# Kernel tuning notes

Measured on AMD Instinct MI355X. Metric: run time of the kernel, lower is better.

## Reference

```python
import jax, jax.numpy as jnp
import numpy as np

N_PTS = 8192   # collocation points (original used 50; scaled up)
N_PARA = 5000  # rows of para, matching the source script
HID = 50


def setup_inputs() -> dict:
    key = jax.random.key(0)
    ks = jax.random.split(key, 10)
    x = jax.random.normal(ks[0], (N_PTS, 3), jnp.float32)
    # para = cat(normal(-2,1) [P,2], normal(0.5,1) [P,1]) as in source script
    a_b = jax.random.normal(ks[1], (N_PARA, 2), jnp.float32) * 1.0 - 2.0
    c = jax.random.normal(ks[2], (N_PARA, 1), jnp.float32) * 1.0 + 0.5
    para = jnp.concatenate([a_b, c], axis=1)

    def init(k, fan_in, shape):
        bound = 1.0 / np.sqrt(fan_in)  # torch Linear default init range
        return jax.random.uniform(k, shape, jnp.float32, -bound, bound)

    W_in = init(ks[3], 3, (3, HID))
    b_in = init(ks[4], 3, (HID,))
    W_hid = init(ks[5], HID, (4, HID, HID))
    b_hid = init(ks[6], HID, (4, HID))
    W_out = init(ks[7], HID, (HID, 2))
    b_out = init(ks[8], HID, (2,))
    return dict(x=x, para=para, W_in=W_in, b_in=b_in, W_hid=W_hid,
                b_hid=b_hid, W_out=W_out, b_out=b_out)


def reference(x, para, W_in, b_in, W_hid, b_hid, W_out, b_out):
    def net(xi):  # xi: [3] -> [2] (u, v)
        h = jnp.tanh(xi @ W_in + b_in)
        for i in range(W_hid.shape[0]):
            h = jnp.tanh(h @ W_hid[i] + b_hid[i])
        return h @ W_out + b_out

    uv = jax.vmap(net)(x)                    # [N, 2]
    jac = jax.vmap(jax.jacrev(net))(x)       # [N, 2, 3]
    hess = jax.vmap(jax.hessian(net))(x)     # [N, 2, 3, 3]

    u, v = uv[:, 0], uv[:, 1]
    u_t, v_t = jac[:, 0, 2], jac[:, 1, 2]
    u_xx, u_yy = hess[:, 0, 0, 0], hess[:, 0, 1, 1]
    v_xx, v_yy = hess[:, 1, 0, 0], hess[:, 1, 1, 1]

    Q = u * u + v * v  # |q|^2
    # f_2 = u_t + 0.5 v_xx + 0.5 a v_yy - 0.5 u_yy + Q v - Q c u + u
    # f_1 = v_t - 0.5 u_xx - 0.5 a u_yy - 0.5 v_yy - Q u - Q c v + v
    base2 = u_t + 0.5 * v_xx - 0.5 * u_yy + Q * v + u   # a,c-independent part
    base1 = v_t - 0.5 * u_xx - 0.5 * v_yy - Q * u + v

    a = para[:, 0:1]   # [P, 1]; column 1 (b) is unused, as in source
    cc = para[:, 2:3]

    f1 = base1[None, :] - 0.5 * a * u_yy[None, :] - cc * (Q * v)[None, :]  # [P, N]
    f2 = base2[None, :] + 0.5 * a * v_yy[None, :] - cc * (Q * u)[None, :]

    # per-row loss: MSE(f1, 0) + MSE(f2, 0)
    return jnp.mean(f1 * f1, axis=1) + jnp.mean(f2 * f2, axis=1)  # [P]
```

## Files before the change

kernel.cpp:

```cpp
#include <hip/hip_runtime.h>
#include <math.h>

#define HID 50
#define NPTS 8192
#define NPARA 5000
#define NLAYERS 4

typedef float f32x4 __attribute__((ext_vector_type(4)));
typedef short short8 __attribute__((ext_vector_type(8)));

union U4S8 { uint4 u; short8 s; };

#define WS_PART 0
#define WS_FRAG 32768
#define WS_WIN  98304
#define WS_BIN  99072
#define WS_BH   99328
#define WS_WOUT 100352
#define WS_NEED 100864

#define S_STRIDE 21
#define S_COMP   (64*S_STRIDE)
#define S_WORDS  (6*S_COMP)

__device__ __forceinline__ float fast_tanh(float x) {
    const float ax = __builtin_fabsf(x);
    const float e  = __expf(2.0f * ax);
    const float r  = __builtin_amdgcn_rcpf(e + 1.0f);
    const float t  = fmaf(-2.0f, r, 1.0f);
    return __builtin_copysignf(t, x);
}

__device__ __forceinline__ void split_bf16(float x, unsigned &hi, unsigned &lo) {
    const unsigned u = __float_as_uint(x);
    const unsigned h = u & 0xFFFF0000u;
    const float rem  = x - __uint_as_float(h);
    const unsigned r = __float_as_uint(rem);
    hi = h >> 16;
    lo = (r + 0x7FFFu + ((r >> 16) & 1u)) >> 16;
}

__device__ __forceinline__ uint4 pack8(const unsigned v[8]) {
    return make_uint4(v[0] | (v[1] << 16), v[2] | (v[3] << 16),
                      v[4] | (v[5] << 16), v[6] | (v[7] << 16));
}

__global__ __launch_bounds__(256) void prep_kernel(
    const float* __restrict__ W_in, const float* __restrict__ b_in,
    const float* __restrict__ W_hid, const float* __restrict__ b_hid,
    const float* __restrict__ W_out, char* __restrict__ wsbase)
{
    const int gid = blockIdx.x * 256 + threadIdx.x;
    if (gid < 2048) {
        const int fid = gid >> 6, lane = gid & 63;
        const int l = fid >> 3, c = (fid >> 2) & 1, t = fid & 3;
        const int q = lane >> 4, n = lane & 15;
        const int gn = t*16 + n;
        unsigned hi[8], lo[8];
        #pragma unroll
        for (int jj = 0; jj < 8; ++jj) {
            const int k = c*32 + q*8 + jj;
            const float w = (k < HID && gn < HID) ? W_hid[(l*HID + k)*HID + gn] : 0.f;
            split_bf16(w, hi[jj], lo[jj]);
        }
        uint4* frag = (uint4*)(wsbase + WS_FRAG);
        frag[(fid*2 + 0)*64 + lane] = pack8(hi);
        frag[(fid*2 + 1)*64 + lane] = pack8(lo);
    } else if (gid < 2240) {
        const int i = gid - 2048, d = i >> 6, j = i & 63;
        ((float*)(wsbase + WS_WIN))[i] = (j < HID) ? W_in[d*HID + j] : 0.f;
    } else if (gid < 2304) {
        const int j = gid - 2240;
        ((float*)(wsbase + WS_BIN))[j] = (j < HID) ? b_in[j] : 0.f;
    } else if (gid < 2560) {
        const int i = gid - 2304, l = i >> 6, j = i & 63;
        ((float*)(wsbase + WS_BH))[i] = (j < HID) ? b_hid[l*HID + j] : 0.f;
    } else if (gid < 2688) {
        const int i = gid - 2560, j = i >> 1, s = i & 1;
        ((float*)(wsbase + WS_WOUT))[i] = (j < HID) ? W_out[j*2 + s] : 0.f;
    }
}

__global__ __launch_bounds__(64) void point_mfma_kernel(
    const float* __restrict__ x,
    const float* __restrict__ b_out,
    const char* __restrict__ wsbase,
    double* __restrict__ part)
{
    __shared__ float S[S_WORDS];
    const int lane = threadIdx.x;
    const int q = lane >> 4, L = lane & 15;

    const float* Winp = (const float*)(wsbase + WS_WIN);
    const float* binp = (const float*)(wsbase + WS_BIN);
    const float* bhp  = (const float*)(wsbase + WS_BH);
    const float* wop  = (const float*)(wsbase + WS_WOUT);
    const uint4* frag = (const uint4*)(wsbase + WS_FRAG);

    const int pid = blockIdx.x * 16 + L;
    const float x0 = x[3*pid+0], x1 = x[3*pid+1], x2 = x[3*pid+2];
    #pragma unroll
    for (int jj = 0; jj < 16; ++jj) {
        const int j = 4*jj + q;
        const float w0 = Winp[j], w1 = Winp[64 + j], w2 = Winp[128 + j];
        const float z  = fmaf(x0, w0, fmaf(x1, w1, fmaf(x2, w2, binp[j])));
        const float h  = fast_tanh(z);
        const float s  = 1.f - h*h;
        const float g  = -2.f*h*s;
        const int base = j*S_STRIDE + L;
        S[0*S_COMP + base] = h;
        S[1*S_COMP + base] = s*w0;
        S[2*S_COMP + base] = s*w1;
        S[3*S_COMP + base] = s*w2;
        S[4*S_COMP + base] = g*w0*w0;
        S[5*S_COMP + base] = g*w1*w1;
    }

    #pragma unroll 1
    for (int l = 0; l < NLAYERS; ++l) {
        f32x4 acc[6][4];
        #pragma unroll
        for (int comp = 0; comp < 6; ++comp)
            #pragma unroll
            for (int t = 0; t < 4; ++t)
                acc[comp][t] = (f32x4){0.f, 0.f, 0.f, 0.f};

        #pragma unroll
        for (int c = 0; c < 2; ++c) {
            uint4 Bh[4], Bl[4];
            #pragma unroll
            for (int t = 0; t < 4; ++t) {
                const int fi = (l*2 + c)*4 + t;
                Bh[t] = frag[(fi*2 + 0)*64 + lane];
                Bl[t] = frag[(fi*2 + 1)*64 + lane];
            }
            #pragma unroll
            for (int comp = 0; comp < 6; ++comp) {
                unsigned hi[8], lo[8];
                #pragma unroll
                for (int jj = 0; jj < 8; ++jj) {
                    const int k = c*32 + q*8 + jj;
                    const float e = S[comp*S_COMP + k*S_STRIDE + L];
                    split_bf16(e, hi[jj], lo[jj]);
                }
                U4S8 Ah, Al;
                Ah.u = pack8(hi);
                Al.u = pack8(lo);
                #pragma unroll
                for (int t = 0; t < 4; ++t) {
                    U4S8 bh, bl;
                    bh.u = Bh[t]; bl.u = Bl[t];
                    acc[comp][t] = __builtin_amdgcn_mfma_f32_16x16x32_bf16(Ah.s, bh.s, acc[comp][t], 0, 0, 0);
                    acc[comp][t] = __builtin_amdgcn_mfma_f32_16x16x32_bf16(Ah.s, bl.s, acc[comp][t], 0, 0, 0);
                    acc[comp][t] = __builtin_amdgcn_mfma_f32_16x16x32_bf16(Al.s, bh.s, acc[comp][t], 0, 0, 0);
                }
            }
        }

        #pragma unroll
        for (int t = 0; t < 4; ++t) {
            const int j = t*16 + L;
            const float bias = bhp[l*64 + j];
            #pragma unroll
            for (int r = 0; r < 4; ++r) {
                const int p = 4*q + r;
                const float za  = acc[0][t][r] + bias;
                const float zx  = acc[1][t][r];
                const float zy  = acc[2][t][r];
                const float zt  = acc[3][t][r];
                const float zxx = acc[4][t][r];
                const float zyy = acc[5][t][r];
                const float h = fast_tanh(za);
                const float s = 1.f - h*h;
                const float g = -2.f*h*s;
                const int base = j*S_STRIDE + p;
                S[0*S_COMP + base] = h;
                S[1*S_COMP + base] = s*zx;
                S[2*S_COMP + base] = s*zy;
                S[3*S_COMP + base] = s*zt;
                S[4*S_COMP + base] = fmaf(g*zx, zx, s*zxx);
                S[5*S_COMP + base] = fmaf(g*zy, zy, s*zyy);
            }
        }
    }

    float du=0.f, dv=0.f, dut=0.f, dvt=0.f, duxx=0.f, dvxx=0.f, duyy=0.f, dvyy=0.f;
    #pragma unroll
    for (int jj = 0; jj < 16; ++jj) {
        const int j = q*16 + jj;
        const float w0 = wop[j*2 + 0], w1 = wop[j*2 + 1];
        const float sh  = S[0*S_COMP + j*S_STRIDE + L];
        const float st_ = S[3*S_COMP + j*S_STRIDE + L];
        const float sxx = S[4*S_COMP + j*S_STRIDE + L];
        const float syy = S[5*S_COMP + j*S_STRIDE + L];
        du   = fmaf(sh,  w0, du);   dv   = fmaf(sh,  w1, dv);
        dut  = fmaf(st_, w0, dut);  dvt  = fmaf(st_, w1, dvt);
        duxx = fmaf(sxx, w0, duxx); dvxx = fmaf(sxx, w1, dvxx);
        duyy = fmaf(syy, w0, duyy); dvyy = fmaf(syy, w1, dvyy);
    }
    #pragma unroll
    for (int off = 16; off <= 32; off <<= 1) {
        du   += __shfl_xor(du,   off); dv   += __shfl_xor(dv,   off);
        dut  += __shfl_xor(dut,  off); dvt  += __shfl_xor(dvt,  off);
        duxx += __shfl_xor(duxx, off); dvxx += __shfl_xor(dvxx, off);
        duyy += __shfl_xor(duyy, off); dvyy += __shfl_xor(dvyy, off);
    }
    const float u = du + b_out[0];
    const float v = dv + b_out[1];
    const float Q = u*u + v*v;
    const float g1 = dvt - 0.5f*duxx - 0.5f*dvyy - Q*u + v;
    const float g2 = dut + 0.5f*dvxx - 0.5f*duyy + Q*v + u;
    const float h1 = 0.5f*duyy, h2 = 0.5f*dvyy;
    const float k1 = Q*v,       k2 = Q*u;

    const double m = (lane < 16) ? 1.0 : 0.0;
    double a0 = m * ((double)g1*(double)g1 + (double)g2*(double)g2);
    double a1 = m * ((double)h1*(double)h1 + (double)h2*(double)h2);
    double a2 = m * ((double)k1*(double)k1 + (double)k2*(double)k2);
    double a3 = m * ((double)g2*(double)h2 - (double)g1*(double)h1);
    double a4 = m * ((double)g1*(double)k1 + (double)g2*(double)k2);
    double a5 = m * ((double)h1*(double)k1 - (double)h2*(double)k2);
    #pragma unroll
    for (int off = 1; off <= 8; off <<= 1) {
        a0 += __shfl_xor(a0, off); a1 += __shfl_xor(a1, off);
        a2 += __shfl_xor(a2, off); a3 += __shfl_xor(a3, off);
        a4 += __shfl_xor(a4, off); a5 += __shfl_xor(a5, off);
    }
    if (lane == 0) {
        double* o = &part[blockIdx.x * 6];
        o[0] = a0; o[1] = a1; o[2] = a2; o[3] = a3; o[4] = a4; o[5] = a5;
    }
}

#define BLOCK_F 1024
#define WPB_F   16
#define GRID_F  512
#define SWIN_SZ (3*HID + 16)
#define SBIN_SZ (HID + 16)
#define SWH_SZ  (NLAYERS*HID*HID + 16)
#define SBH_SZ  (NLAYERS*HID + 16)
#define SWO_SZ  (2*64)

__device__ __forceinline__ float readlane_f(float v, int k) {
    return __int_as_float(__builtin_amdgcn_readlane(__float_as_int(v), k));
}

__global__ __launch_bounds__(BLOCK_F, 8) void point_fallback_kernel(
    const float* __restrict__ x,
    const float* __restrict__ W_in, const float* __restrict__ b_in,
    const float* __restrict__ W_hid, const float* __restrict__ b_hid,
    const float* __restrict__ W_out, const float* __restrict__ b_out,
    double* __restrict__ part, int use_atomic)
{
    __shared__ float sWin[SWIN_SZ];
    __shared__ float sbin[SBIN_SZ];
    __shared__ float sWh[SWH_SZ];
    __shared__ float sbh[SBH_SZ];
    __shared__ float sWo[SWO_SZ];
    __shared__ float sbo[2];
    __shared__ double sRed[WPB_F][6];

    const int tid = threadIdx.x;
    for (int i = tid; i < 3*HID; i += BLOCK_F) sWin[i] = W_in[i];
    for (int i = 3*HID + tid; i < SWIN_SZ; i += BLOCK_F) sWin[i] = 0.f;
    for (int i = tid; i < HID; i += BLOCK_F) sbin[i] = b_in[i];
    for (int i = HID + tid; i < SBIN_SZ; i += BLOCK_F) sbin[i] = 0.f;
    for (int i = tid; i < NLAYERS*HID*HID; i += BLOCK_F) sWh[i] = W_hid[i];
    for (int i = NLAYERS*HID*HID + tid; i < SWH_SZ; i += BLOCK_F) sWh[i] = 0.f;
    for (int i = tid; i < NLAYERS*HID; i += BLOCK_F) sbh[i] = b_hid[i];
    for (int i = NLAYERS*HID + tid; i < SBH_SZ; i += BLOCK_F) sbh[i] = 0.f;
    for (int i = tid; i < 2*HID; i += BLOCK_F) sWo[i] = W_out[i];
    for (int i = 2*HID + tid; i < SWO_SZ; i += BLOCK_F) sWo[i] = 0.f;
    if (tid < 2) sbo[tid] = b_out[tid];
    __syncthreads();

    const int lane = tid & 63;
    const int wave = tid >> 6;
    const int p    = blockIdx.x * WPB_F + wave;

    const float x0 = x[3*p+0], x1 = x[3*p+1], x2 = x[3*p+2];
    const float w0 = sWin[lane];
    const float w1 = sWin[HID + lane];
    const float w2 = sWin[2*HID + lane];
    float z = fmaf(x0, w0, fmaf(x1, w1, fmaf(x2, w2, sbin[lane])));
    float h = fast_tanh(z);
    float s = 1.f - h*h;
    float hx = s*w0, hy = s*w1, ht = s*w2;
    float hxx = -2.f*h*s*w0*w0;
    float hyy = -2.f*h*s*w1*w1;

    for (int l = 0; l < NLAYERS; ++l) {
        const float* __restrict__ Wl = &sWh[l*HID*HID];
        float za  = sbh[l*HID + lane];
        float zx = 0.f, zy = 0.f, zt = 0.f, zxx = 0.f, zyy = 0.f;
        #pragma unroll
        for (int k = 0; k < HID; ++k) {
            const float w = Wl[k*HID + lane];
            za  = fmaf(readlane_f(h,   k), w, za);
            zx  = fmaf(readlane_f(hx,  k), w, zx);
            zy  = fmaf(readlane_f(hy,  k), w, zy);
            zt  = fmaf(readlane_f(ht,  k), w, zt);
            zxx = fmaf(readlane_f(hxx, k), w, zxx);
            zyy = fmaf(readlane_f(hyy, k), w, zyy);
        }
        const float hn = fast_tanh(za);
        const float sn = 1.f - hn*hn;
        hxx = fmaf(sn, zxx, -2.f*hn*sn*zx*zx);
        hyy = fmaf(sn, zyy, -2.f*hn*sn*zy*zy);
        hx = sn*zx; hy = sn*zy; ht = sn*zt;
        h = hn;
    }

    const float wo0 = sWo[lane*2+0];
    const float wo1 = sWo[lane*2+1];
    const bool act = (lane < HID);
    float pu   = act ? h  *wo0 : 0.f;
    float pv   = act ? h  *wo1 : 0.f;
    float put  = act ? ht *wo0 : 0.f;
    float pvt  = act ? ht *wo1 : 0.f;
    float puxx = act ? hxx*wo0 : 0.f;
    float pvxx = act ? hxx*wo1 : 0.f;
    float puyy = act ? hyy*wo0 : 0.f;
    float pvyy = act ? hyy*wo1 : 0.f;
    #pragma unroll
    for (int off = 32; off > 0; off >>= 1) {
        pu   += __shfl_xor(pu,   off);
        pv   += __shfl_xor(pv,   off);
        put  += __shfl_xor(put,  off);
        pvt  += __shfl_xor(pvt,  off);
        puxx += __shfl_xor(puxx, off);
        pvxx += __shfl_xor(pvxx, off);
        puyy += __shfl_xor(puyy, off);
        pvyy += __shfl_xor(pvyy, off);
    }
    const float u = pu + sbo[0];
    const float v = pv + sbo[1];
    const float Q = u*u + v*v;
    const float g1 = pvt - 0.5f*puxx - 0.5f*pvyy - Q*u + v;
    const float g2 = put + 0.5f*pvxx - 0.5f*puyy + Q*v + u;
    const float h1 = 0.5f*puyy, h2 = 0.5f*pvyy;
    const float k1 = Q*v,       k2 = Q*u;

    const double a0 = (double)g1*(double)g1 + (double)g2*(double)g2;
    const double a1 = (double)h1*(double)h1 + (double)h2*(double)h2;
    const double a2 = (double)k1*(double)k1 + (double)k2*(double)k2;
    const double a3 = (double)g2*(double)h2 - (double)g1*(double)h1;
    const double a4 = (double)g1*(double)k1 + (double)g2*(double)k2;
    const double a5 = (double)h1*(double)k1 - (double)h2*(double)k2;

    if (lane == 0) {
        sRed[wave][0] = a0; sRed[wave][1] = a1; sRed[wave][2] = a2;
        sRed[wave][3] = a3; sRed[wave][4] = a4; sRed[wave][5] = a5;
    }
    __syncthreads();
    if (tid < 6) {
        double t = 0.0;
        #pragma unroll
        for (int wv = 0; wv < WPB_F; ++wv) t += sRed[wv][tid];
        if (use_atomic) atomicAdd(&part[tid], t);
        else            part[blockIdx.x * 6 + tid] = t;
    }
}

__global__ __launch_bounds__(512) void para_kernel(
    const float* __restrict__ para,
    const double* __restrict__ part, int nsets,
    float* __restrict__ out)
{
    __shared__ double sW[8][6];
    __shared__ double sS[6];
    const int tid  = threadIdx.x;
    const int lane = tid & 63;
    const int wave = tid >> 6;

    double c0=0,c1=0,c2=0,c3=0,c4=0,c5=0;
    for (int i = tid; i < nsets; i += 512) {
        const double* qp = &part[i*6];
        c0 += qp[0]; c1 += qp[1]; c2 += qp[2]; c3 += qp[3]; c4 += qp[4]; c5 += qp[5];
    }
    #pragma unroll
    for (int off = 32; off > 0; off >>= 1) {
        c0 += __shfl_xor(c0, off); c1 += __shfl_xor(c1, off);
        c2 += __shfl_xor(c2, off); c3 += __shfl_xor(c3, off);
        c4 += __shfl_xor(c4, off); c5 += __shfl_xor(c5, off);
    }
    if (lane == 0) {
        sW[wave][0]=c0; sW[wave][1]=c1; sW[wave][2]=c2;
        sW[wave][3]=c3; sW[wave][4]=c4; sW[wave][5]=c5;
    }
    __syncthreads();
    if (tid < 6) {
        double t = 0.0;
        #pragma unroll
        for (int wv = 0; wv < 8; ++wv) t += sW[wv][tid];
        sS[tid] = t;
    }
    __syncthreads();

    const double S0=sS[0], S1=sS[1], S2=sS[2], S3=sS[3], S4=sS[4], S5=sS[5];
    for (int p = blockIdx.x * 512 + tid; p < NPARA; p += gridDim.x * 512) {
        const double a  = (double)para[3*p+0];
        const double cc = (double)para[3*p+2];
        const double r = S0 + a*a*S1 + cc*cc*S2 + 2.0*a*S3 - 2.0*cc*S4 + 2.0*a*cc*S5;
        out[p] = (float)(r * (1.0 / (double)NPTS));
    }
}

extern "C" void kernel_launch(void* const* d_in, const int* in_sizes, int n_in,
                              void* d_out, int out_size, void* d_ws, size_t ws_size,
                              hipStream_t stream) {
    const float* x     = (const float*)d_in[0];
    const float* para  = (const float*)d_in[1];
    const float* W_in  = (const float*)d_in[2];
    const float* b_in  = (const float*)d_in[3];
    const float* W_hid = (const float*)d_in[4];
    const float* b_hid = (const float*)d_in[5];
    const float* W_out = (const float*)d_in[6];
    const float* b_out = (const float*)d_in[7];

    char*   wsbase = (char*)d_ws;
    double* part   = (double*)d_ws;

    if (ws_size >= (size_t)WS_NEED) {
        prep_kernel<<<11, 256, 0, stream>>>(W_in, b_in, W_hid, b_hid, W_out, wsbase);
        point_mfma_kernel<<<512, 64, 0, stream>>>(x, b_out, wsbase, part);
        para_kernel<<<10, 512, 0, stream>>>(para, part, 512, (float*)d_out);
    } else if (ws_size >= (size_t)(GRID_F * 6 * sizeof(double))) {
        point_fallback_kernel<<<GRID_F, BLOCK_F, 0, stream>>>(
            x, W_in, b_in, W_hid, b_hid, W_out, b_out, part, 0);
        para_kernel<<<10, 512, 0, stream>>>(para, part, GRID_F, (float*)d_out);
    } else {
        hipMemsetAsync(part, 0, 6*sizeof(double), stream);
        point_fallback_kernel<<<GRID_F, BLOCK_F, 0, stream>>>(
            x, W_in, b_in, W_hid, b_hid, W_out, b_out, part, 1);
        para_kernel<<<10, 512, 0, stream>>>(para, part, 1, (float*)d_out);
    }
}
```

Before: 93.97 us.

## Split MLP layer tiles across two waves and store pre-split bf16 activations

The point kernel now runs two waves per block. Each wave computes half of the 64 output columns per layer, with block barriers between the shared-memory read and write phases. Activations are stored in shared memory already split into packed bf16 hi/lo pairs, so MFMA operands are built with byte permutes instead of running the split at read time. The aim is to halve each wave's serial MFMA and tanh chain and double the number of waves in this small grid. In exchange it adds __syncthreads barriers, makes both waves read all A operands, and adds a cross-wave shared-memory reduction at the end.

New measurement: 89.02 us. -5.3%, faster.

```diff
diff --git a/kernel.cpp b/kernel.cpp
--- a/kernel.cpp
+++ b/kernel.cpp
@@ -23,6 +23,9 @@
 #define S_COMP   (64*S_STRIDE)
 #define S_WORDS  (6*S_COMP)
 
+#define SEL_HI 0x05040100u
+#define SEL_LO 0x07060302u
+
 __device__ __forceinline__ float fast_tanh(float x) {
     const float ax = __builtin_fabsf(x);
     const float e  = __expf(2.0f * ax);
@@ -38,6 +41,16 @@
     const unsigned r = __float_as_uint(rem);
     hi = h >> 16;
     lo = (r + 0x7FFFu + ((r >> 16) & 1u)) >> 16;
+}
+
+__device__ __forceinline__ unsigned pack_split(float x) {
+    unsigned hi, lo;
+    split_bf16(x, hi, lo);
+    return hi | (lo << 16);
+}
+
+__device__ __forceinline__ float unpack_sum(unsigned w) {
+    return __uint_as_float(w << 16) + __uint_as_float(w & 0xFFFF0000u);
 }
 
 __device__ __forceinline__ uint4 pack8(const unsigned v[8]) {
@@ -81,14 +94,18 @@
     }
 }
 
-__global__ __launch_bounds__(64) void point_mfma_kernel(
+__global__ __launch_bounds__(128, 1) void point_mfma_kernel(
     const float* __restrict__ x,
     const float* __restrict__ b_out,
     const char* __restrict__ wsbase,
     double* __restrict__ part)
 {
-    __shared__ float S[S_WORDS];
-    const int lane = threadIdx.x;
+    __shared__ unsigned S[S_WORDS];
+    __shared__ float xd[16][8];
+
+    const int tid  = threadIdx.x;
+    const int wave = tid >> 6;
+    const int lane = tid & 63;
     const int q = lane >> 4, L = lane & 15;
 
     const float* Winp = (const float*)(wsbase + WS_WIN);
@@ -100,99 +117,116 @@
     const int pid = blockIdx.x * 16 + L;
     const float x0 = x[3*pid+0], x1 = x[3*pid+1], x2 = x[3*pid+2];
     #pragma unroll
-    for (int jj = 0; jj < 16; ++jj) {
-        const int j = 4*jj + q;
+    for (int jj = 0; jj < 8; ++jj) {
+        const int j = 32*wave + 8*q + jj;
         const float w0 = Winp[j], w1 = Winp[64 + j], w2 = Winp[128 + j];
         const float z  = fmaf(x0, w0, fmaf(x1, w1, fmaf(x2, w2, binp[j])));
         const float h  = fast_tanh(z);
         const float s  = 1.f - h*h;
         const float g  = -2.f*h*s;
         const int base = j*S_STRIDE + L;
-        S[0*S_COMP + base] = h;
-        S[1*S_COMP + base] = s*w0;
-        S[2*S_COMP + base] = s*w1;
-        S[3*S_COMP + base] = s*w2;
-        S[4*S_COMP + base] = g*w0*w0;
-        S[5*S_COMP + base] = g*w1*w1;
-    }
+        S[0*S_COMP + base] = pack_split(h);
+        S[1*S_COMP + base] = pack_split(s*w0);
+        S[2*S_COMP + base] = pack_split(s*w1);
+        S[3*S_COMP + base] = pack_split(s*w2);
+        S[4*S_COMP + base] = pack_split(g*w0*w0);
+        S[5*S_COMP + base] = pack_split(g*w1*w1);
+    }
+    __syncthreads();
 
     #pragma unroll 1
     for (int l = 0; l < NLAYERS; ++l) {
-        f32x4 acc[6][4];
+        uint4 Bh[2][2], Bl[2][2];
+        #pragma unroll
+        for (int c = 0; c < 2; ++c)
+            #pragma unroll
+            for (int tt = 0; tt < 2; ++tt) {
+                const int fi = (l*2 + c)*4 + (2*wave + tt);
+                Bh[c][tt] = frag[(fi*2 + 0)*64 + lane];
+                Bl[c][tt] = frag[(fi*2 + 1)*64 + lane];
+            }
+
+        uint4 Ah[2][6], Al[2][6];
+        #pragma unroll
+        for (int c = 0; c < 2; ++c)
+            #pragma unroll
+            for (int comp = 0; comp < 6; ++comp) {
+                const int base = comp*S_COMP + (c*32 + q*8)*S_STRIDE + L;
+                unsigned w[8];
+                #pragma unroll
+                for (int jj = 0; jj < 8; ++jj) w[jj] = S[base + jj*S_STRIDE];
+                Ah[c][comp] = make_uint4(
+                    __builtin_amdgcn_perm(w[1], w[0], SEL_HI),
+                    __builtin_amdgcn_perm(w[3], w[2], SEL_HI),
+                    __builtin_amdgcn_perm(w[5], w[4], SEL_HI),
+                    __builtin_amdgcn_perm(w[7], w[6], SEL_HI));
+                Al[c][comp] = make_uint4(
+                    __builtin_amdgcn_perm(w[1], w[0], SEL_LO),
+                    __builtin_amdgcn_perm(w[3], w[2], SEL_LO),
+                    __builtin_amdgcn_perm(w[5], w[4], SEL_LO),
+                    __builtin_amdgcn_perm(w[7], w[6], SEL_LO));
+            }
+        __syncthreads();
+
+        f32x4 acc[6][2];
         #pragma unroll
         for (int comp = 0; comp < 6; ++comp)
             #pragma unroll
-            for (int t = 0; t < 4; ++t)
-                acc[comp][t] = (f32x4){0.f, 0.f, 0.f, 0.f};
-
-        #pragma unroll
-        for (int c = 0; c < 2; ++c) {
-            uint4 Bh[4], Bl[4];
-            #pragma unroll
-            for (int t = 0; t < 4; ++t) {
-                const int fi = (l*2 + c)*4 + t;
-                Bh[t] = frag[(fi*2 + 0)*64 + lane];
-                Bl[t] = frag[(fi*2 + 1)*64 + lane];
-            }
+            for (int tt = 0; tt < 2; ++tt)
+                acc[comp][tt] = (f32x4){0.f, 0.f, 0.f, 0.f};
+
+        #pragma unroll
+        for (int c = 0; c < 2; ++c)
             #pragma unroll
             for (int comp = 0; comp < 6; ++comp) {
-                unsigned hi[8], lo[8];
+                U4S8 ah, al; ah.u = Ah[c][comp]; al.u = Al[c][comp];
                 #pragma unroll
-                for (int jj = 0; jj < 8; ++jj) {
-                    const int k = c*32 + q*8 + jj;
-                    const float e = S[comp*S_COMP + k*S_STRIDE + L];
-                    split_bf16(e, hi[jj], lo[jj]);
-                }
-                U4S8 Ah, Al;
-                Ah.u = pack8(hi);
-                Al.u = pack8(lo);
-                #pragma unroll
-                for (int t = 0; t < 4; ++t) {
-                    U4S8 bh, bl;
-                    bh.u = Bh[t]; bl.u = Bl[t];
-                    acc[comp][t] = __builtin_amdgcn_mfma_f32_16x16x32_bf16(Ah.s, bh.s, acc[comp][t], 0, 0, 0);
-                    acc[comp][t] = __builtin_amdgcn_mfma_f32_16x16x32_bf16(Ah.s, bl.s, acc[comp][t], 0, 0, 0);
-                    acc[comp][t] = __builtin_amdgcn_mfma_f32_16x16x32_bf16(Al.s, bh.s, acc[comp][t], 0, 0, 0);
+                for (int tt = 0; tt < 2; ++tt) {
+                    U4S8 bh, bl; bh.u = Bh[c][tt]; bl.u = Bl[c][tt];
+                    acc[comp][tt] = __builtin_amdgcn_mfma_f32_16x16x32_bf16(ah.s, bh.s, acc[comp][tt], 0, 0, 0);
+                    acc[comp][tt] = __builtin_amdgcn_mfma_f32_16x16x32_bf16(ah.s, bl.s, acc[comp][tt], 0, 0, 0);
+                    acc[comp][tt] = __builtin_amdgcn_mfma_f32_16x16x32_bf16(al.s, bh.s, acc[comp][tt], 0, 0, 0);
                 }
             }
-        }
-
-        #pragma unroll
-        for (int t = 0; t < 4; ++t) {
-            const int j = t*16 + L;
+
+        #pragma unroll
+        for (int tt = 0; tt < 2; ++tt) {
+            const int j = (2*wave + tt)*16 + L;
             const float bias = bhp[l*64 + j];
             #pragma unroll
             for (int r = 0; r < 4; ++r) {
                 const int p = 4*q + r;
-                const float za  = acc[0][t][r] + bias;
-                const float zx  = acc[1][t][r];
-                const float zy  = acc[2][t][r];
-                const float zt  = acc[3][t][r];
-                const float zxx = acc[4][t][r];
-                const float zyy = acc[5][t][r];
+                const float za  = acc[0][tt][r] + bias;
+                const float zx  = acc[1][tt][r];
+                const float zy  = acc[2][tt][r];
+                const float zt  = acc[3][tt][r];
+                const float zxx = acc[4][tt][r];
+                const float zyy = acc[5][tt][r];
                 const float h = fast_tanh(za);
                 const float s = 1.f - h*h;
                 const float g = -2.f*h*s;
                 const int base = j*S_STRIDE + p;
-                S[0*S_COMP + base] = h;
-                S[1*S_COMP + base] = s*zx;
-                S[2*S_COMP + base] = s*zy;
-                S[3*S_COMP + base] = s*zt;
-                S[4*S_COMP + base] = fmaf(g*zx, zx, s*zxx);
-                S[5*S_COMP + base] = fmaf(g*zy, zy, s*zyy);
+                S[0*S_COMP + base] = pack_split(h);
+                S[1*S_COMP + base] = pack_split(s*zx);
+                S[2*S_COMP + base] = pack_split(s*zy);
+                S[3*S_COMP + base] = pack_split(s*zt);
+                S[4*S_COMP + base] = pack_split(fmaf(g*zx, zx, s*zxx));
+                S[5*S_COMP + base] = pack_split(fmaf(g*zy, zy, s*zyy));
             }
         }
+        __syncthreads();
     }
 
     float du=0.f, dv=0.f, dut=0.f, dvt=0.f, duxx=0.f, dvxx=0.f, duyy=0.f, dvyy=0.f;
     #pragma unroll
-    for (int jj = 0; jj < 16; ++jj) {
-        const int j = q*16 + jj;
+    for (int jj = 0; jj < 8; ++jj) {
+        const int j = 32*wave + 8*q + jj;
+        const int base = j*S_STRIDE + L;
+        const float sh  = unpack_sum(S[0*S_COMP + base]);
+        const float st_ = unpack_sum(S[3*S_COMP + base]);
+        const float sxx = unpack_sum(S[4*S_COMP + base]);
+        const float syy = unpack_sum(S[5*S_COMP + base]);
         const float w0 = wop[j*2 + 0], w1 = wop[j*2 + 1];
-        const float sh  = S[0*S_COMP + j*S_STRIDE + L];
-        const float st_ = S[3*S_COMP + j*S_STRIDE + L];
-        const float sxx = S[4*S_COMP + j*S_STRIDE + L];
-        const float syy = S[5*S_COMP + j*S_STRIDE + L];
         du   = fmaf(sh,  w0, du);   dv   = fmaf(sh,  w1, dv);
         dut  = fmaf(st_, w0, dut);  dvt  = fmaf(st_, w1, dvt);
         duxx = fmaf(sxx, w0, duxx); dvxx = fmaf(sxx, w1, dvxx);
@@ -205,30 +239,40 @@
         duxx += __shfl_xor(duxx, off); dvxx += __shfl_xor(dvxx, off);
         duyy += __shfl_xor(duyy, off); dvyy += __shfl_xor(dvyy, off);
     }
-    const float u = du + b_out[0];
-    const float v = dv + b_out[1];
-    const float Q = u*u + v*v;
-    const float g1 = dvt - 0.5f*duxx - 0.5f*dvyy - Q*u + v;
-    const float g2 = dut + 0.5f*dvxx - 0.5f*duyy + Q*v + u;
-    const float h1 = 0.5f*duyy, h2 = 0.5f*dvyy;
-    const float k1 = Q*v,       k2 = Q*u;
-
-    const double m = (lane < 16) ? 1.0 : 0.0;
-    double a0 = m * ((double)g1*(double)g1 + (double)g2*(double)g2);
-    double a1 = m * ((double)h1*(double)h1 + (double)h2*(double)h2);
-    double a2 = m * ((double)k1*(double)k1 + (double)k2*(double)k2);
-    double a3 = m * ((double)g2*(double)h2 - (double)g1*(double)h1);
-    double a4 = m * ((double)g1*(double)k1 + (double)g2*(double)k2);
-    double a5 = m * ((double)h1*(double)k1 - (double)h2*(double)k2);
-    #pragma unroll
-    for (int off = 1; off <= 8; off <<= 1) {
-        a0 += __shfl_xor(a0, off); a1 += __shfl_xor(a1, off);
-        a2 += __shfl_xor(a2, off); a3 += __shfl_xor(a3, off);
-        a4 += __shfl_xor(a4, off); a5 += __shfl_xor(a5, off);
-    }
-    if (lane == 0) {
-        double* o = &part[blockIdx.x * 6];
-        o[0] = a0; o[1] = a1; o[2] = a2; o[3] = a3; o[4] = a4; o[5] = a5;
+    if (wave == 1 && lane < 16) {
+        xd[lane][0]=du;   xd[lane][1]=dv;   xd[lane][2]=dut;  xd[lane][3]=dvt;
+        xd[lane][4]=duxx; xd[lane][5]=dvxx; xd[lane][6]=duyy; xd[lane][7]=dvyy;
+    }
+    __syncthreads();
+    if (wave == 0) {
+        du   += xd[L][0]; dv   += xd[L][1]; dut  += xd[L][2]; dvt  += xd[L][3];
+        duxx += xd[L][4]; dvxx += xd[L][5]; duyy += xd[L][6]; dvyy += xd[L][7];
+
+        const float u = du + b_out[0];
+        const float v = dv + b_out[1];
+        const float Q = u*u + v*v;
+        const float g1 = dvt - 0.5f*duxx - 0.5f*dvyy - Q*u + v;
+        const float g2 = dut + 0.5f*dvxx - 0.5f*duyy + Q*v + u;
+        const float h1 = 0.5f*duyy, h2 = 0.5f*dvyy;
+        const float k1 = Q*v,       k2 = Q*u;
+
+        const double m = (lane < 16) ? 1.0 : 0.0;
+        double a0 = m * ((double)g1*(double)g1 + (double)g2*(double)g2);
+        double a1 = m * ((double)h1*(double)h1 + (double)h2*(double)h2);
+        double a2 = m * ((double)k1*(double)k1 + (double)k2*(double)k2);
+        double a3 = m * ((double)g2*(double)h2 - (double)g1*(double)h1);
+        double a4 = m * ((double)g1*(double)k1 + (double)g2*(double)k2);
+        double a5 = m * ((double)h1*(double)k1 - (double)h2*(double)k2);
+        #pragma unroll
+        for (int off = 1; off <= 32; off <<= 1) {
+            a0 += __shfl_xor(a0, off); a1 += __shfl_xor(a1, off);
+            a2 += __shfl_xor(a2, off); a3 += __shfl_xor(a3, off);
+            a4 += __shfl_xor(a4, off); a5 += __shfl_xor(a5, off);
+        }
+        if (lane == 0) {
+            double* o = &part[blockIdx.x * 6];
+            o[0] = a0; o[1] = a1; o[2] = a2; o[3] = a3; o[4] = a4; o[5] = a5;
+        }
     }
 }
 
@@ -423,7 +467,7 @@
 
     if (ws_size >= (size_t)WS_NEED) {
         prep_kernel<<<11, 256, 0, stream>>>(W_in, b_in, W_hid, b_hid, W_out, wsbase);
-        point_mfma_kernel<<<512, 64, 0, stream>>>(x, b_out, wsbase, part);
+        point_mfma_kernel<<<512, 128, 0, stream>>>(x, b_out, wsbase, part);
         para_kernel<<<10, 512, 0, stream>>>(para, part, 512, (float*)d_out);
     } else if (ws_size >= (size_t)(GRID_F * 6 * sizeof(double))) {
         point_fallback_kernel<<<GRID_F, BLOCK_F, 0, stream>>>(
```
